# Performance work log

Hardware: AMD Instinct MI355X
Metric: run time of the kernel (lower is better)

The kernel has to match this reference:

```python
import jax, jax.numpy as jnp
import numpy as np

SIZE_MIN, SIZE_MAX = 10.0, 40.0
CROP = 28


def convert_to_box_list(x):
    # [B, C, W, H] -> [W*H, B, C]
    b, c, w, h = x.shape
    return jnp.transpose(x, (2, 3, 0, 1)).reshape(w * h, b, c)


def invert_convert_to_box_list(x, w, h):
    # [W*H, B, C] -> [B, C, W, H]
    n, b, c = x.shape
    return jnp.transpose(x.reshape(w, h, b, c), (2, 3, 0, 1))


def bilinear_sample(img, x, y):
    # img: [C, W, H]; x, y: pixel coords of shape S -> [C, *S]; zero outside.
    C, W, H = img.shape
    x0 = jnp.floor(x); y0 = jnp.floor(y)
    x1 = x0 + 1.0; y1 = y0 + 1.0
    wx1 = x - x0; wx0 = 1.0 - wx1
    wy1 = y - y0; wy0 = 1.0 - wy1
    def fetch(xi, yi):
        valid = ((xi >= 0) & (xi < W) & (yi >= 0) & (yi < H)).astype(img.dtype)
        xc = jnp.clip(xi, 0, W - 1).astype(jnp.int32)
        yc = jnp.clip(yi, 0, H - 1).astype(jnp.int32)
        return img[:, xc, yc] * valid
    return (fetch(x0, y0) * (wx0 * wy0) + fetch(x1, y0) * (wx1 * wy0)
            + fetch(x0, y1) * (wx0 * wy1) + fetch(x1, y1) * (wx1 * wy1))


def crop(bx, by, bw, bh, big, ws, hs):
    # bx..bh: [k, B]; big: [B, C, W, H] -> [k, B, C, ws, hs]
    u = (jnp.arange(ws) + 0.5) / ws
    v = (jnp.arange(hs) + 0.5) / hs
    xs = bx[..., None] - 0.5 * bw[..., None] + u * bw[..., None] - 0.5  # [k,B,ws]
    ys = by[..., None] - 0.5 * bh[..., None] + v * bh[..., None] - 0.5  # [k,B,hs]
    def one(xr, yr, img):
        X = jnp.broadcast_to(xr[:, None], (ws, hs))
        Y = jnp.broadcast_to(yr[None, :], (ws, hs))
        return bilinear_sample(img, X, Y)
    return jax.vmap(jax.vmap(one, (0, 0, 0)), (0, 0, None))(xs, ys, big)


def uncrop(bx, by, bw, bh, small, Wb, Hb):
    # small: [k, B, C, ws, hs] -> [k, B, C, Wb, Hb] (zero outside each box)
    ws, hs = small.shape[-2], small.shape[-1]
    Xc = jnp.arange(Wb) + 0.5
    Yc = jnp.arange(Hb) + 0.5
    xs = (Xc - (bx[..., None] - 0.5 * bw[..., None])) / bw[..., None] * ws - 0.5
    ys = (Yc - (by[..., None] - 0.5 * bh[..., None])) / bh[..., None] * hs - 0.5
    def one(xr, yr, img):
        X = jnp.broadcast_to(xr[:, None], (Wb, Hb))
        Y = jnp.broadcast_to(yr[None, :], (Wb, Hb))
        return bilinear_sample(img, X, Y)
    return jax.vmap(jax.vmap(one, (0, 0, 0)), (0, 0, 0))(xs, ys, small)


def tmaps_to_bb(tmaps, W_raw, H_raw):
    # tmaps: [B, 4, nw, nh] in (0,1) -> box lists [n_all, B]
    nw, nh = tmaps.shape[-2], tmaps.shape[-1]
    tx, ty, tw, th = tmaps[:, 0], tmaps[:, 1], tmaps[:, 2], tmaps[:, 3]
    ix = jnp.arange(nw, dtype=tmaps.dtype)[:, None]
    iy = jnp.arange(nh, dtype=tmaps.dtype)[None, :]
    bx_map = W_raw * (ix + tx) / nw
    by_map = H_raw * (iy + ty) / nh
    bw_map = SIZE_MIN + (SIZE_MAX - SIZE_MIN) * tw
    bh_map = SIZE_MIN + (SIZE_MAX - SIZE_MIN) * th
    tolist = lambda m: convert_to_box_list(m[:, None]).squeeze(-1)
    return tolist(bx_map), tolist(by_map), tolist(bw_map), tolist(bh_map)


def forward_core(logit_mu, zwhere_mu, zwhere_std, eps_zwhere, eps_zinstance,
                 features, w_zwhere, b_zwhere, w_enc, b_enc, w_dec, b_dec, n_objects_max):
    B, Cf, W_raw, H_raw = features.shape
    nw, nh = logit_mu.shape[-2], logit_mu.shape[-1]

    # zwhere posterior sample + KL vs N(0,1)
    zwhere_sample_map = zwhere_mu + zwhere_std * eps_zwhere
    zwhere_kl_map = 0.5 * (zwhere_mu ** 2 + zwhere_std ** 2) - jnp.log(zwhere_std) - 0.5

    # decode zwhere (1x1 conv) -> sigmoid tmaps -> boxes
    tmaps = jax.nn.sigmoid(jnp.einsum('bzwh,cz->bcwh', zwhere_sample_map, w_zwhere)
                           + b_zwhere[None, :, None, None])
    bx_all, by_all, bw_all, bh_all = tmaps_to_bb(tmaps, W_raw, H_raw)

    area_all = bw_all * bh_all
    area_map = invert_convert_to_box_list(area_all[..., None], nw, nh)

    # c sample = logit map (deterministic relaxation of the DPP/Bernoulli sample)
    c_sample_map = logit_mu
    prob_map = jax.nn.sigmoid(c_sample_map)
    c_all = convert_to_box_list(c_sample_map).squeeze(-1)   # [n_all, B]
    prob_all = convert_to_box_list(prob_map).squeeze(-1)

    # top-k per batch element (indices constant wrt grads)
    k = min(n_objects_max, c_all.shape[0])
    idx = jax.lax.stop_gradient(jax.lax.top_k(c_all.T, k)[1].T)  # [k, B]
    take = lambda t: jnp.take_along_axis(t, idx, axis=0)
    c_few, prob_few = take(c_all), take(prob_all)
    bx_few, by_few, bw_few, bh_few = take(bx_all), take(by_all), take(bw_all), take(bh_all)

    zwhere_sample_all = convert_to_box_list(zwhere_sample_map)  # [n_all, B, Z]
    zwhere_kl_all = convert_to_box_list(zwhere_kl_map)
    idx_z = idx[..., None]
    zwhere_sample_few = jnp.take_along_axis(zwhere_sample_all, idx_z, axis=0)
    zwhere_kl_few = jnp.take_along_axis(zwhere_kl_all, idx_z, axis=0)

    # crop full-res features at the k boxes -> [k, B, Cf, CROP, CROP]
    cropped = crop(bx_few, by_few, bw_few, bh_few, features, CROP, CROP)

    # encoder zinstance (flatten + linear -> mu, std)
    flat = cropped.reshape(k, B, -1)
    enc = jnp.einsum('kbf,df->kbd', flat, w_enc) + b_enc
    dim_z = enc.shape[-1] // 2
    zi_mu = enc[..., :dim_z]
    zi_std = jax.nn.softplus(enc[..., dim_z:]) + 1e-4
    zi_sample = zi_mu + zi_std * eps_zinstance
    zi_kl = 0.5 * (zi_mu ** 2 + zi_std ** 2) - jnp.log(zi_std) - 0.5

    # decoder zinstance (linear -> [k, B, 2, CROP, CROP])
    dec = jnp.einsum('kbz,fz->kbf', zi_sample, w_dec) + b_dec
    raw = dec.reshape(k, B, 2, CROP, CROP)
    small = jnp.concatenate([jax.nn.softplus(raw[..., :1, :, :]),
                             jax.nn.sigmoid(raw[..., 1:, :, :])], axis=-3)

    big_stuff = uncrop(bx_few, by_few, bw_few, bh_few,
                       small * c_few[..., None, None, None], W_raw, H_raw)
    big_weight = big_stuff[..., :1, :, :]
    big_img = big_stuff[..., 1:, :, :]

    # from_weights_to_masks over box dim (dim=-5 of [k,B,1,W,H])
    sum_w = jnp.sum(big_weight, axis=0, keepdims=True)
    big_mask = jnp.tanh(sum_w) * (big_weight / jnp.maximum(sum_w, 1e-6))
    big_mask_non = jnp.tanh(big_weight)

    return (prob_map, area_map, c_few, prob_few, bx_few, by_few, bw_few, bh_few,
            big_mask, big_mask_non, big_img,
            zwhere_sample_few, zwhere_kl_few, zi_sample, zi_kl)


def setup_inputs() -> dict:
    key = jax.random.key(0)
    ks = jax.random.split(key, 9)
    B, NW, NH = 8, 32, 32
    W_RAW = H_RAW = 128
    CF, ZW, ZI, K = 32, 8, 32, 48
    fan_in = CF * CROP * CROP
    return {
        "logit_mu": jax.random.normal(ks[0], (B, 1, NW, NH), jnp.float32),
        "zwhere_mu": 0.5 * jax.random.normal(ks[1], (B, ZW, NW, NH), jnp.float32),
        "zwhere_std": jax.random.uniform(ks[2], (B, ZW, NW, NH), jnp.float32, 0.1, 1.0),
        "eps_zwhere": jax.random.normal(ks[3], (B, ZW, NW, NH), jnp.float32),
        "eps_zinstance": jax.random.normal(ks[4], (K, B, ZI), jnp.float32),
        "features": jax.random.normal(ks[5], (B, CF, W_RAW, H_RAW), jnp.float32),
        "w_zwhere": 0.3 * jax.random.normal(ks[6], (4, ZW), jnp.float32),
        "b_zwhere": jnp.zeros((4,), jnp.float32),
        "w_enc": jax.random.normal(ks[7], (2 * ZI, fan_in), jnp.float32) / np.sqrt(fan_in).astype(np.float32),
        "b_enc": jnp.zeros((2 * ZI,), jnp.float32),
        "w_dec": jax.random.normal(ks[8], (2 * CROP * CROP, ZI), jnp.float32) / np.sqrt(ZI).astype(np.float32),
        "b_dec": jnp.zeros((2 * CROP * CROP,), jnp.float32),
        "n_objects_max": 48,
    }


def reference(logit_mu, zwhere_mu, zwhere_std, eps_zwhere, eps_zinstance, features,
              w_zwhere, b_zwhere, w_enc, b_enc, w_dec, b_dec, n_objects_max):
    return forward_core(logit_mu, zwhere_mu, zwhere_std, eps_zwhere, eps_zinstance,
                        features, w_zwhere, b_zwhere, w_enc, b_enc, w_dec, b_dec,
                        n_objects_max)
```

## Files before the change

### kernel.cpp

```cpp
#include <hip/hip_runtime.h>
#include <math.h>

#define B 8
#define NWD 32
#define NHD 32
#define NBOX 1024
#define ZWD 8
#define ZID 32
#define KOBJ 48
#define CFEAT 32
#define WRAW 128
#define HRAW 128
#define CR 28
#define CR2 784
#define FAN 25088
#define KB 384

#define OFF_PROB   0
#define OFF_AREA   8192
#define OFF_CFEW   16384
#define OFF_PFEW   16768
#define OFF_BXF    17152
#define OFF_BYF    17536
#define OFF_BWF    17920
#define OFF_BHF    18304
#define OFF_BMASK  18688
#define OFF_BMASKN 6310144
#define OFF_BIMG   12601600
#define OFF_ZWS    18893056
#define OFF_ZWK    18896128
#define OFF_ZIS    18899200
#define OFF_ZIK    18911488

#define WS_SMALL 32768

#define SCR_PART 0
#define SCR_WT   2752512

#define FSPLIT 49
#define FPB 512
#define CHK 128
#define NCH 4
#define MKB 16
#define KSTR 152
#define TAPN (MKB*28)

typedef __attribute__((ext_vector_type(8))) short bfrag;
typedef __attribute__((ext_vector_type(4))) float f32x4;

__device__ __forceinline__ float sigm(float x){ return 1.0f/(1.0f+expf(-x)); }
__device__ __forceinline__ float softpl(float x){ return fmaxf(x,0.0f) + log1pf(expf(-fabsf(x))); }
__device__ __forceinline__ float ftanh(float x){
  float t = __expf(2.0f*x);
  return 1.0f - __fdividef(2.0f, t + 1.0f);
}
__device__ __forceinline__ unsigned short f2bf(float f){
  unsigned u = __float_as_uint(f);
  unsigned r = u + 0x7FFFu + ((u >> 16) & 1u);
  return (unsigned short)(r >> 16);
}
__device__ __forceinline__ unsigned okey(float f){
  unsigned b = __float_as_uint(f);
  return b ^ ((b & 0x80000000u) ? 0xFFFFFFFFu : 0x80000000u);
}

__global__ __launch_bounds__(256) void prep_kernel(
    const float* __restrict__ wenc, unsigned short* __restrict__ wt,
    const float* __restrict__ logit, const float* __restrict__ zmu,
    const float* __restrict__ zstd, const float* __restrict__ zeps,
    const float* __restrict__ wz, const float* __restrict__ bz,
    float* __restrict__ out){
  __shared__ __align__(16) unsigned su[NBOX];
  if (blockIdx.x < 784){
    const int ks = blockIdx.x;
    const int tid = threadIdx.x;
    const int lane = tid & 63;
    const int t = tid >> 6;
    const int d = t*16 + (lane & 15);
    const int k0 = ks*32 + (lane >> 4)*8;
    const float* src = wenc + (size_t)d*FAN + k0;
    float4 a = *(const float4*)src;
    float4 b = *(const float4*)(src + 4);
    unsigned long long p0 = (unsigned long long)f2bf(a.x)
      | ((unsigned long long)f2bf(a.y) << 16)
      | ((unsigned long long)f2bf(a.z) << 32)
      | ((unsigned long long)f2bf(a.w) << 48);
    unsigned long long p1 = (unsigned long long)f2bf(b.x)
      | ((unsigned long long)f2bf(b.y) << 16)
      | ((unsigned long long)f2bf(b.z) << 32)
      | ((unsigned long long)f2bf(b.w) << 48);
    unsigned short* dst = wt + ((size_t)ks*256 + tid)*8;
    *(unsigned long long*)dst       = p0;
    *(unsigned long long*)(dst + 4) = p1;
    return;
  }
  const int bid = blockIdx.x - 784;
  const int b  = bid >> 2;
  const int sb = bid & 3;
  const int tid = threadIdx.x;
  #pragma unroll
  for (int u = 0; u < 4; u++){
    int j = tid + u*256;
    su[j] = okey(logit[b*NBOX + j]);
  }
  const int n = sb*256 + tid;
  const int w = n >> 5, h = n & 31;
  float acc0=bz[0], acc1=bz[1], acc2=bz[2], acc3=bz[3];
  #pragma unroll
  for(int z=0; z<ZWD; z++){
    int id = ((b*ZWD + z)*NWD + w)*NHD + h;
    float s = zmu[id] + zstd[id]*zeps[id];
    acc0 += s*wz[0*ZWD+z]; acc1 += s*wz[1*ZWD+z];
    acc2 += s*wz[2*ZWD+z]; acc3 += s*wz[3*ZWD+z];
  }
  float tx=sigm(acc0), ty=sigm(acc1), tw=sigm(acc2), th=sigm(acc3);
  float bx = (128.0f*((float)w + tx))/32.0f;
  float by = (128.0f*((float)h + ty))/32.0f;
  float bwv = 10.0f + 30.0f*tw;
  float bhv = 10.0f + 30.0f*th;
  float lg = logit[b*NBOX + n];
  out[OFF_PROB + b*NBOX + n] = sigm(lg);
  out[OFF_AREA + b*NBOX + n] = bwv*bhv;
  __syncthreads();
  const unsigned ui = su[n];
  const uint4* su4 = (const uint4*)su;
  int rank = 0;
  #pragma unroll 4
  for (int jq = 0; jq < NBOX/4; jq++){
    uint4 v = su4[jq];
    int j = jq*4;
    rank += (v.x > ui || (v.x == ui && j   < n)) ? 1 : 0;
    rank += (v.y > ui || (v.y == ui && j+1 < n)) ? 1 : 0;
    rank += (v.z > ui || (v.z == ui && j+2 < n)) ? 1 : 0;
    rank += (v.w > ui || (v.w == ui && j+3 < n)) ? 1 : 0;
  }
  if (rank < KOBJ){
    out[OFF_CFEW + rank*B + b] = lg;
    out[OFF_PFEW + rank*B + b] = sigm(lg);
    out[OFF_BXF  + rank*B + b] = bx;
    out[OFF_BYF  + rank*B + b] = by;
    out[OFF_BWF  + rank*B + b] = bwv;
    out[OFF_BHF  + rank*B + b] = bhv;
    #pragma unroll
    for(int z=0; z<ZWD; z++){
      int id = ((b*ZWD + z)*NWD + w)*NHD + h;
      float mu = zmu[id], sd = zstd[id];
      out[OFF_ZWS + (rank*B+b)*ZWD + z] = mu + sd*zeps[id];
      out[OFF_ZWK + (rank*B+b)*ZWD + z] = 0.5f*(mu*mu + sd*sd) - logf(sd) - 0.5f;
    }
  }
}

__global__ __launch_bounds__(256, 4) void enc_kernel(
    const float* __restrict__ feat, const unsigned short* __restrict__ wt,
    const float* __restrict__ outc, float* __restrict__ part){
  __shared__ __align__(16) unsigned short cl0[MKB*KSTR];
  __shared__ __align__(16) unsigned short cl1[MKB*KSTR];
  __shared__ float2 wxs[TAPN]; __shared__ int2 xos[TAPN];
  __shared__ float2 wys[TAPN]; __shared__ int2 yos[TAPN];
  __shared__ float rAx[MKB], rSx[MKB], rAy[MKB], rSy[MKB];
  const int tid = threadIdx.x;
  const int fs  = blockIdx.x % FSPLIT;
  const int kb0 = (blockIdx.x / FSPLIT) * MKB;
  if (tid < MKB){
    float bx = outc[OFF_BXF + kb0 + tid];
    float by = outc[OFF_BYF + kb0 + tid];
    float bw = outc[OFF_BWF + kb0 + tid];
    float bh = outc[OFF_BHF + kb0 + tid];
    float sx = bw * (1.0f/(float)CR), sy = bh * (1.0f/(float)CR);
    rSx[tid] = sx; rSy[tid] = sy;
    rAx[tid] = bx - 0.5f*bw + 0.5f*sx - 0.5f;
    rAy[tid] = by - 0.5f*bh + 0.5f*sy - 0.5f;
  }
  __syncthreads();
  #pragma unroll
  for (int it = 0; it < 4; it++){
    int idx = it*256 + tid;
    if (idx < 2*TAPN){
      int isy = idx >= TAPN;
      int q = idx - (isy ? TAPN : 0);
      int rr = q / 28, i = q - rr*28;
      float A = isy ? rAy[rr] : rAx[rr];
      float S = isy ? rSy[rr] : rSx[rr];
      float x = fmaf((float)i, S, A);
      float x0f = floorf(x); int x0 = (int)x0f;
      float w1 = x - x0f, w0 = 1.0f - w1;
      if ((unsigned)x0     >= WRAW) w0 = 0.f;
      if ((unsigned)(x0+1) >= WRAW) w1 = 0.f;
      int c0 = min(max(x0,0),WRAW-1), c1 = min(max(x0+1,0),WRAW-1);
      if (isy){ wys[q] = make_float2(w0,w1); yos[q] = make_int2(c0, c1); }
      else    { wxs[q] = make_float2(w0,w1); xos[q] = make_int2(c0*HRAW, c1*HRAW); }
    }
  }
  __syncthreads();
  float raw[8][4];
  int ji[8];
  const int fblk = fs*FPB;
  #define GATHER(CH) { \
    _Pragma("unroll") \
    for (int u = 0; u < 8; u++){ \
      int idx = u*256 + tid; \
      int rr = idx >> 7, ff = idx & 127; \
      int f = fblk + (CH)*CHK + ff; \
      int c = f / CR2; int p = f - c*CR2; \
      int i = p / CR;  int j = p - i*CR; \
      int ii = rr*28 + i, jj = rr*28 + j; \
      ji[u] = (jj << 16) | ii; \
      int2 xo = xos[ii]; int2 yo = yos[jj]; \
      const float* img = feat + (size_t)((rr & (B-1))*CFEAT + c)*(WRAW*HRAW); \
      raw[u][0] = img[xo.x + yo.x]; \
      raw[u][1] = img[xo.x + yo.y]; \
      raw[u][2] = img[xo.y + yo.x]; \
      raw[u][3] = img[xo.y + yo.y]; \
    } }
  #define STORE(DST) { \
    _Pragma("unroll") \
    for (int u = 0; u < 8; u++){ \
      int idx = u*256 + tid; \
      int rr = idx >> 7, ff = idx & 127; \
      int ii = ji[u] & 0xffff, jj = ji[u] >> 16; \
      float2 wx = wxs[ii]; float2 wy = wys[jj]; \
      float v = (raw[u][0]*wy.x + raw[u][1]*wy.y)*wx.x \
              + (raw[u][2]*wy.x + raw[u][3]*wy.y)*wx.y; \
      (DST)[rr*KSTR + ff] = f2bf(v); \
    } }
  GATHER(0);
  STORE(cl0);
  __syncthreads();
  const int lane = tid & 63, wv = tid >> 6;
  const int lr = lane & 15, lg = lane >> 4;
  f32x4 acc = {0.f,0.f,0.f,0.f};
  #pragma unroll
  for (int ch = 0; ch < NCH; ch++){
    unsigned short* cur = (ch & 1) ? cl1 : cl0;
    unsigned short* nxt = (ch & 1) ? cl0 : cl1;
    const unsigned short* bptr = wt + (size_t)(fs*16 + ch*4)*2048 + wv*512 + lane*8;
    bfrag b0 = *(const bfrag*)(bptr);
    bfrag b1 = *(const bfrag*)(bptr + 2048);
    bfrag b2 = *(const bfrag*)(bptr + 4096);
    bfrag b3 = *(const bfrag*)(bptr + 6144);
    if (ch < NCH-1){ GATHER(ch+1); }
    const unsigned short* arow = &cur[lr*KSTR + lg*8];
    bfrag a0 = *(const bfrag*)(arow);
    bfrag a1 = *(const bfrag*)(arow + 32);
    bfrag a2 = *(const bfrag*)(arow + 64);
    bfrag a3 = *(const bfrag*)(arow + 96);
    acc = __builtin_amdgcn_mfma_f32_16x16x32_bf16(a0, b0, acc, 0, 0, 0);
    acc = __builtin_amdgcn_mfma_f32_16x16x32_bf16(a1, b1, acc, 0, 0, 0);
    acc = __builtin_amdgcn_mfma_f32_16x16x32_bf16(a2, b2, acc, 0, 0, 0);
    acc = __builtin_amdgcn_mfma_f32_16x16x32_bf16(a3, b3, acc, 0, 0, 0);
    if (ch < NCH-1){ STORE(nxt); }
    __syncthreads();
  }
  float* dst = part + ((size_t)fs*KB + kb0)*64;
  #pragma unroll
  for (int r = 0; r < 4; r++){
    int row = lg*4 + r;
    dst[row*64 + wv*16 + lr] = acc[r];
  }
  #undef GATHER
  #undef STORE
}

__global__ __launch_bounds__(256) void zi_dec_kernel(
    const float* __restrict__ part, const float* __restrict__ benc,
    const float* __restrict__ ieps, const float* __restrict__ wdec,
    const float* __restrict__ bdec, float* __restrict__ out,
    float* __restrict__ ws){
  int kb = blockIdx.x;
  int d = threadIdx.x & 63, seg = threadIdx.x >> 6;
  float s0=0.f, s1=0.f;
  for (int f = seg; f < FSPLIT; f += 8)
    s0 += part[((size_t)f*KB + kb)*64 + d];
  for (int f = seg+4; f < FSPLIT; f += 8)
    s1 += part[((size_t)f*KB + kb)*64 + d];
  __shared__ float red[4][64];
  __shared__ float zs[ZID];
  __shared__ float cf_s;
  red[seg][d] = s0 + s1;
  __syncthreads();
  if (threadIdx.x < ZID){
    int dd = threadIdx.x;
    float mu = benc[dd]     + red[0][dd]     + red[1][dd]     + red[2][dd]     + red[3][dd];
    float pe = benc[ZID+dd] + red[0][ZID+dd] + red[1][ZID+dd] + red[2][ZID+dd] + red[3][ZID+dd];
    float sd = softpl(pe) + 1e-4f;
    float zsv = mu + sd*ieps[kb*ZID + dd];
    out[OFF_ZIS + kb*ZID + dd] = zsv;
    out[OFF_ZIK + kb*ZID + dd] = 0.5f*(mu*mu + sd*sd) - logf(sd) - 0.5f;
    zs[dd] = zsv;
  }
  if (threadIdx.x == 0) cf_s = out[OFF_CFEW + kb];
  __syncthreads();
  float cf = cf_s;
  for (int f = threadIdx.x; f < 2*CR2; f += 256){
    float a = bdec[f];
    #pragma unroll
    for (int q = 0; q < 8; q++){
      float4 w4 = *(const float4*)&wdec[f*ZID + q*4];
      a = fmaf(zs[q*4+0], w4.x, a);
      a = fmaf(zs[q*4+1], w4.y, a);
      a = fmaf(zs[q*4+2], w4.z, a);
      a = fmaf(zs[q*4+3], w4.w, a);
    }
    float v = (f < CR2) ? softpl(a) : sigm(a);
    ws[WS_SMALL + (size_t)kb*(2*CR2) + f] = v*cf;
  }
}

__global__ __launch_bounds__(256) void uncrop_compose_kernel(
    const float* __restrict__ ws, float* __restrict__ out){
  const int t = blockIdx.x*256 + threadIdx.x;
  const int b = t >> 14, p = t & 16383;
  const int X = p >> 7, Y = p & 127;
  __shared__ float sAx[KOBJ], sSx[KOBJ], sAy[KOBJ], sSy[KOBJ];
  if (threadIdx.x < KOBJ){
    int k = threadIdx.x;
    float bx = out[OFF_BXF + k*B + b], bw = out[OFF_BWF + k*B + b];
    float by = out[OFF_BYF + k*B + b], bh = out[OFF_BHF + k*B + b];
    float ix = __fdividef((float)CR, bw), iy = __fdividef((float)CR, bh);
    sSx[k] = ix; sAx[k] = (0.5f*bw - bx)*ix - 0.5f;
    sSy[k] = iy; sAy[k] = (0.5f*bh - by)*iy - 0.5f;
  }
  __syncthreads();
  const float xc = (float)X + 0.5f, yc = (float)Y + 0.5f;
  float wr[KOBJ];
  float sum = 0.f;
  #pragma unroll
  for (int k = 0; k < KOBJ; k++){
    float x = fmaf(xc, sSx[k], sAx[k]);
    float y = fmaf(yc, sSy[k], sAy[k]);
    const float* sm = ws + WS_SMALL + (size_t)(k*B + b)*(2*CR2);
    float x0f = floorf(x), y0f = floorf(y);
    int x0 = (int)x0f, y0 = (int)y0f;
    float wx1 = x - x0f, wx0 = 1.0f - wx1;
    float wy1 = y - y0f, wy0 = 1.0f - wy1;
    if ((unsigned)x0     >= CR) wx0 = 0.f;
    if ((unsigned)(x0+1) >= CR) wx1 = 0.f;
    if ((unsigned)y0     >= CR) wy0 = 0.f;
    if ((unsigned)(y0+1) >= CR) wy1 = 0.f;
    int x0c = min(max(x0,0),CR-1), x1c = min(max(x0+1,0),CR-1);
    int y0c = min(max(y0,0),CR-1), y1c = min(max(y0+1,0),CR-1);
    const float* r0 = sm + x0c*CR;
    const float* r1 = sm + x1c*CR;
    float v0 = (r0[y0c]*wy0 + r0[y1c]*wy1)*wx0 + (r1[y0c]*wy0 + r1[y1c]*wy1)*wx1;
    const float* q0 = r0 + CR2;
    const float* q1 = r1 + CR2;
    float v1 = (q0[y0c]*wy0 + q0[y1c]*wy1)*wx0 + (q1[y0c]*wy0 + q1[y1c]*wy1)*wx1;
    wr[k] = v0; sum += v0;
    out[OFF_BIMG + (size_t)(k*B + b)*16384 + p] = v1;
  }
  float th = ftanh(sum);
  float inv = 1.0f / fmaxf(sum, 1e-6f);
  #pragma unroll
  for (int k = 0; k < KOBJ; k++){
    size_t o = (size_t)(k*B + b)*16384 + p;
    out[OFF_BMASK  + o] = th * (wr[k] * inv);
    out[OFF_BMASKN + o] = ftanh(wr[k]);
  }
}

extern "C" void kernel_launch(void* const* d_in, const int* in_sizes, int n_in,
                              void* d_out, int out_size, void* d_ws, size_t ws_size,
                              hipStream_t stream) {
  (void)in_sizes; (void)n_in; (void)out_size; (void)ws_size;
  const float* logit = (const float*)d_in[0];
  const float* zmu   = (const float*)d_in[1];
  const float* zstd  = (const float*)d_in[2];
  const float* zeps  = (const float*)d_in[3];
  const float* ieps  = (const float*)d_in[4];
  const float* feat  = (const float*)d_in[5];
  const float* wz    = (const float*)d_in[6];
  const float* bz    = (const float*)d_in[7];
  const float* wenc  = (const float*)d_in[8];
  const float* benc  = (const float*)d_in[9];
  const float* wdec  = (const float*)d_in[10];
  const float* bdec  = (const float*)d_in[11];
  float* out = (float*)d_out;
  float* ws  = (float*)d_ws;
  float* scr = out + OFF_BMASK;
  float* part = scr + SCR_PART;
  unsigned short* wt = (unsigned short*)(scr + SCR_WT);

  prep_kernel         <<<784 + B*4, 256, 0, stream>>>(wenc, wt, logit, zmu, zstd, zeps, wz, bz, out);
  enc_kernel          <<<(KB/MKB)*FSPLIT, 256, 0, stream>>>(feat, wt, out, part);
  zi_dec_kernel       <<<KB, 256, 0, stream>>>(part, benc, ieps, wdec, bdec, out, ws);
  uncrop_compose_kernel<<<(B*WRAW*HRAW)/256, 256, 0, stream>>>(ws, out);
}
```

Before: 92.46 us.

## Pre-pack features as bf16 Y-neighbour pairs to halve bilinear gather loads

The prep kernel gains 2048 extra blocks that convert the feature map to bf16 and store each pixel together with its y+1 neighbour, so one 32-bit load fetches both vertical taps. The encoder gather then issues two loads per sample instead of four fp32 loads, and the y-offset table shrinks to a single base index, with weights shifted for the left border. In exchange it adds an 8 MB pre-pass write and read, and the sampled values lose precision because the features are rounded to bf16 before interpolation.

```diff
diff --git a/kernel.cpp b/kernel.cpp
--- a/kernel.cpp
+++ b/kernel.cpp
@@ -35,7 +35,8 @@
 #define WS_SMALL 32768
 
 #define SCR_PART 0
-#define SCR_WT   2752512
+#define SCR_WT   1204224
+#define SCR_F2Y  2007040
 
 #define FSPLIT 49
 #define FPB 512
@@ -66,6 +67,7 @@
 
 __global__ __launch_bounds__(256) void prep_kernel(
     const float* __restrict__ wenc, unsigned short* __restrict__ wt,
+    const float* __restrict__ feat, unsigned short* __restrict__ f2y,
     const float* __restrict__ logit, const float* __restrict__ zmu,
     const float* __restrict__ zstd, const float* __restrict__ zeps,
     const float* __restrict__ wz, const float* __restrict__ bz,
@@ -94,7 +96,22 @@
     *(unsigned long long*)(dst + 4) = p1;
     return;
   }
-  const int bid = blockIdx.x - 784;
+  if (blockIdx.x < 784 + 2048){
+    const int t0 = ((blockIdx.x - 784)*256 + threadIdx.x)*8;
+    const int bc = t0 >> 14;
+    const int rem = t0 & 16383;
+    const int X = rem >> 7, Y0 = rem & 127;
+    const float* row = feat + ((size_t)bc << 14) + (X << 7);
+    unsigned short* dst = f2y + (size_t)t0*2;
+    #pragma unroll
+    for (int e = 0; e < 8; e++){
+      int Y = Y0 + e;
+      dst[e*2]   = f2bf(row[Y]);
+      dst[e*2+1] = f2bf(row[min(Y+1,127)]);
+    }
+    return;
+  }
+  const int bid = blockIdx.x - (784 + 2048);
   const int b  = bid >> 2;
   const int sb = bid & 3;
   const int tid = threadIdx.x;
@@ -152,12 +169,12 @@
 }
 
 __global__ __launch_bounds__(256, 4) void enc_kernel(
-    const float* __restrict__ feat, const unsigned short* __restrict__ wt,
+    const unsigned short* __restrict__ f2y, const unsigned short* __restrict__ wt,
     const float* __restrict__ outc, float* __restrict__ part){
   __shared__ __align__(16) unsigned short cl0[MKB*KSTR];
   __shared__ __align__(16) unsigned short cl1[MKB*KSTR];
   __shared__ float2 wxs[TAPN]; __shared__ int2 xos[TAPN];
-  __shared__ float2 wys[TAPN]; __shared__ int2 yos[TAPN];
+  __shared__ float2 wys[TAPN]; __shared__ int   yos[TAPN];
   __shared__ float rAx[MKB], rSx[MKB], rAy[MKB], rSy[MKB];
   const int tid = threadIdx.x;
   const int fs  = blockIdx.x % FSPLIT;
@@ -187,13 +204,18 @@
       float w1 = x - x0f, w0 = 1.0f - w1;
       if ((unsigned)x0     >= WRAW) w0 = 0.f;
       if ((unsigned)(x0+1) >= WRAW) w1 = 0.f;
-      int c0 = min(max(x0,0),WRAW-1), c1 = min(max(x0+1,0),WRAW-1);
-      if (isy){ wys[q] = make_float2(w0,w1); yos[q] = make_int2(c0, c1); }
-      else    { wxs[q] = make_float2(w0,w1); xos[q] = make_int2(c0*HRAW, c1*HRAW); }
+      if (isy){
+        if (x0 < 0){ w0 = w1; w1 = 0.f; }
+        int yb = min(max(x0,0), HRAW-1);
+        wys[q] = make_float2(w0,w1); yos[q] = yb;
+      } else {
+        int c0 = min(max(x0,0),WRAW-1), c1 = min(max(x0+1,0),WRAW-1);
+        wxs[q] = make_float2(w0,w1); xos[q] = make_int2(c0<<7, c1<<7);
+      }
     }
   }
   __syncthreads();
-  float raw[8][4];
+  unsigned raw0[8], raw1[8];
   int ji[8];
   const int fblk = fs*FPB;
   #define GATHER(CH) { \
@@ -206,12 +228,10 @@
       int i = p / CR;  int j = p - i*CR; \
       int ii = rr*28 + i, jj = rr*28 + j; \
       ji[u] = (jj << 16) | ii; \
-      int2 xo = xos[ii]; int2 yo = yos[jj]; \
-      const float* img = feat + (size_t)((rr & (B-1))*CFEAT + c)*(WRAW*HRAW); \
-      raw[u][0] = img[xo.x + yo.x]; \
-      raw[u][1] = img[xo.x + yo.y]; \
-      raw[u][2] = img[xo.y + yo.x]; \
-      raw[u][3] = img[xo.y + yo.y]; \
+      int2 xo = xos[ii]; int yb = yos[jj]; \
+      int eb = (((rr & (B-1))*CFEAT + c) << 14) + yb; \
+      raw0[u] = *(const unsigned*)&f2y[(size_t)(eb + xo.x)*2]; \
+      raw1[u] = *(const unsigned*)&f2y[(size_t)(eb + xo.y)*2]; \
     } }
   #define STORE(DST) { \
     _Pragma("unroll") \
@@ -220,8 +240,11 @@
       int rr = idx >> 7, ff = idx & 127; \
       int ii = ji[u] & 0xffff, jj = ji[u] >> 16; \
       float2 wx = wxs[ii]; float2 wy = wys[jj]; \
-      float v = (raw[u][0]*wy.x + raw[u][1]*wy.y)*wx.x \
-              + (raw[u][2]*wy.x + raw[u][3]*wy.y)*wx.y; \
+      float p00 = __uint_as_float(raw0[u] << 16); \
+      float p01 = __uint_as_float(raw0[u] & 0xffff0000u); \
+      float p10 = __uint_as_float(raw1[u] << 16); \
+      float p11 = __uint_as_float(raw1[u] & 0xffff0000u); \
+      float v = (p00*wy.x + p01*wy.y)*wx.x + (p10*wy.x + p11*wy.y)*wx.y; \
       (DST)[rr*KSTR + ff] = f2bf(v); \
     } }
   GATHER(0);
@@ -379,10 +402,12 @@
   float* ws  = (float*)d_ws;
   float* scr = out + OFF_BMASK;
   float* part = scr + SCR_PART;
-  unsigned short* wt = (unsigned short*)(scr + SCR_WT);
-
-  prep_kernel         <<<784 + B*4, 256, 0, stream>>>(wenc, wt, logit, zmu, zstd, zeps, wz, bz, out);
-  enc_kernel          <<<(KB/MKB)*FSPLIT, 256, 0, stream>>>(feat, wt, out, part);
+  unsigned short* wt  = (unsigned short*)(scr + SCR_WT);
+  unsigned short* f2y = (unsigned short*)(scr + SCR_F2Y);
+
+  prep_kernel         <<<784 + 2048 + B*4, 256, 0, stream>>>(wenc, wt, feat, f2y,
+                                                             logit, zmu, zstd, zeps, wz, bz, out);
+  enc_kernel          <<<(KB/MKB)*FSPLIT, 256, 0, stream>>>(f2y, wt, out, part);
   zi_dec_kernel       <<<KB, 256, 0, stream>>>(part, benc, ieps, wdec, bdec, out, ws);
   uncrop_compose_kernel<<<(B*WRAW*HRAW)/256, 256, 0, stream>>>(ws, out);
 }
```

Result: slower. 95.26 us (+3.0%).
